# Kernel tuning notes

Hardware: AMD Instinct MI355X
Metric: run time of the kernel (lower is better)

Reference implementation:

```python
import jax, jax.numpy as jnp
import numpy as np

D = 1024
H = 16
FFN = 4096
B = 4
S = 1024
EPS = 1e-12
NEG = -1e9


def _layernorm(x, gamma, beta):
    mean = x.mean(-1, keepdims=True)
    var = ((x - mean) ** 2).mean(-1, keepdims=True)  # biased var, matches unbiased=False
    return gamma * (x - mean) * jax.lax.rsqrt(var + EPS) + beta


def setup_inputs() -> dict:
    key = jax.random.key(0)
    ks = jax.random.split(key, 16)
    s_in = 1.0 / np.sqrt(D)
    s_ff = 1.0 / np.sqrt(FFN)
    return {
        "x": jax.random.normal(ks[0], (B, S, D), dtype=jnp.float32),
        "mask": jax.random.randint(ks[1], (B, H, S), 0, 2) > 0,  # bernoulli(0.5) key mask
        "Wqkv": jax.random.uniform(ks[2], (3 * D, D), minval=-s_in, maxval=s_in),
        "bqkv": jax.random.uniform(ks[3], (3 * D,), minval=-s_in, maxval=s_in),
        "Wo": jax.random.uniform(ks[4], (D, D), minval=-s_in, maxval=s_in),
        "bo": jax.random.uniform(ks[5], (D,), minval=-s_in, maxval=s_in),
        "W1": jax.random.uniform(ks[6], (FFN, D), minval=-s_in, maxval=s_in),
        "b1": jax.random.uniform(ks[7], (FFN,), minval=-s_in, maxval=s_in),
        "W2": jax.random.uniform(ks[8], (D, FFN), minval=-s_ff, maxval=s_ff),
        "b2": jax.random.uniform(ks[9], (D,), minval=-s_ff, maxval=s_ff),
        "g1": jnp.ones((D,), jnp.float32),
        "be1": jnp.zeros((D,), jnp.float32),
        "g2": jnp.ones((D,), jnp.float32),
        "be2": jnp.zeros((D,), jnp.float32),
    }


def reference(x, mask, Wqkv, bqkv, Wo, bo, W1, b1, W2, b2, g1, be1, g2, be2):
    b, s, _ = x.shape
    hd = D // H
    scale = hd ** -0.5

    # --- ProbSparseSelfAttention (dropout in eval mode) ---
    qkv = x @ Wqkv.T + bqkv                                   # [b, s, 3D]
    q, k, v = jnp.split(qkv, 3, axis=-1)
    q = q.reshape(b, s, H, hd).transpose(0, 2, 1, 3)          # [b, h, s, d]
    k = k.reshape(b, s, H, hd).transpose(0, 2, 1, 3)
    v = v.reshape(b, s, H, hd).transpose(0, 2, 1, 3)
    scores = jnp.einsum('bhid,bhjd->bhij', q * scale, k)      # [b, h, s, s]
    scores = jnp.where(mask[:, :, None, :], scores, NEG)      # mask keys (broadcast over i)
    attn = jax.nn.softmax(scores, axis=-1)
    ctx = jnp.einsum('bhij,bhjd->bhid', attn, v)
    ctx = ctx.transpose(0, 2, 1, 3).reshape(b, s, D)
    attn_out = ctx @ Wo.T + bo

    # residual + LayerNorm 1
    h = _layernorm(attn_out + x, g1, be1)

    # --- FFN ---
    ff = jax.nn.relu(h @ W1.T + b1) @ W2.T + b2

    # residual + LayerNorm 2
    return _layernorm(ff + h, g2, be2)
```

## Files before the change

### kernel.cpp

```cpp
#include <hip/hip_runtime.h>

#define DDIM 1024
#define FFN_DIM 4096
#define SS 1024
#define MTOK 4096

typedef __bf16 bf16x8 __attribute__((ext_vector_type(8)));
typedef float f32x4 __attribute__((ext_vector_type(4)));
typedef unsigned short ushort4v __attribute__((ext_vector_type(4)));
typedef unsigned short ushort8v __attribute__((ext_vector_type(8)));

__device__ __forceinline__ unsigned short f2bf(float f) {
    union { float f; unsigned u; } x;
    x.f = f;
    unsigned r = x.u + 0x7FFFu + ((x.u >> 16) & 1u);
    return (unsigned short)(r >> 16);
}

__device__ __forceinline__ int swz(int off) {
    return off ^ ((((off >> 7) & 7) ^ ((off >> 10) & 1)) << 4);
}

__device__ __forceinline__ void gload_lds16(const void* g, void* l) {
    __builtin_amdgcn_global_load_lds(
        (__attribute__((address_space(1))) unsigned int*)(unsigned long long)(g),
        (__attribute__((address_space(3))) unsigned int*)(l), 16, 0, 0);
}

__global__ __launch_bounds__(256) void cvt_bf16(const float* __restrict__ in,
                                                unsigned short* __restrict__ out, int n4) {
    int i = blockIdx.x * 256 + threadIdx.x;
    if (i < n4) {
        float4 v = ((const float4*)in)[i];
        ushort4v u = {f2bf(v.x), f2bf(v.y), f2bf(v.z), f2bf(v.w)};
        ((ushort4v*)out)[i] = u;
    }
}

template <int EPI, int BN>
__global__ __launch_bounds__(256) void gemm_bt(const unsigned short* __restrict__ A,
                                               const unsigned short* __restrict__ B,
                                               const float* __restrict__ bias,
                                               void* __restrict__ Cout,
                                               int M, int N, int K) {
    constexpr int NF = BN / 32;
    __shared__ unsigned short Asm[128 * 32];
    __shared__ unsigned short Bsm[BN * 32];
    const int tid = threadIdx.x;
    const int wid = tid >> 6, lane = tid & 63;
    const int m0 = blockIdx.y * 128, n0 = blockIdx.x * BN;
    const int lr = lane & 15, lk = (lane >> 4) * 8;
    const int wr = (wid >> 1) * 64, wc = (wid & 1) * (BN / 2);

    f32x4 acc[4][NF];
#pragma unroll
    for (int i = 0; i < 4; i++)
#pragma unroll
        for (int j = 0; j < NF; j++) acc[i][j] = (f32x4){0.f, 0.f, 0.f, 0.f};

    const unsigned short* Ag = A + (size_t)m0 * K;
    const unsigned short* Bg = B + (size_t)n0 * K;

    for (int k0 = 0; k0 < K; k0 += 32) {
#pragma unroll
        for (int p = 0; p < 2; ++p) {
            int idx = p * 4096 + wid * 1024 + lane * 16;
            int row = idx >> 6, ce = (idx & 63) >> 1;
            gload_lds16(Ag + (size_t)row * K + k0 + ce, (char*)Asm + p * 4096 + wid * 1024);
        }
#pragma unroll
        for (int p = 0; p < BN / 64; ++p) {
            int idx = p * 4096 + wid * 1024 + lane * 16;
            int row = idx >> 6, ce = (idx & 63) >> 1;
            gload_lds16(Bg + (size_t)row * K + k0 + ce, (char*)Bsm + p * 4096 + wid * 1024);
        }
        __syncthreads();
        bf16x8 af[4], bfr[NF];
#pragma unroll
        for (int m = 0; m < 4; m++) af[m] = *(const bf16x8*)&Asm[(wr + m * 16 + lr) * 32 + lk];
#pragma unroll
        for (int n = 0; n < NF; n++) bfr[n] = *(const bf16x8*)&Bsm[(wc + n * 16 + lr) * 32 + lk];
#pragma unroll
        for (int m = 0; m < 4; m++)
#pragma unroll
            for (int n = 0; n < NF; n++)
                acc[m][n] = __builtin_amdgcn_mfma_f32_16x16x32_bf16(af[m], bfr[n], acc[m][n], 0, 0, 0);
        __syncthreads();
    }

    float bv[NF];
#pragma unroll
    for (int n = 0; n < NF; n++) bv[n] = bias[n0 + wc + n * 16 + lr];
    const int r0 = (lane >> 4) * 4;
#pragma unroll
    for (int m = 0; m < 4; m++) {
#pragma unroll
        for (int n = 0; n < NF; n++) {
            int col = n0 + wc + n * 16 + lr;
#pragma unroll
            for (int r = 0; r < 4; r++) {
                int row = m0 + wr + m * 16 + r0 + r;
                float v = acc[m][n][r] + bv[n];
                if (EPI == 0) {
                    ((float*)Cout)[(size_t)row * N + col] = v;
                } else if (EPI == 1) {
                    ((unsigned short*)Cout)[(size_t)row * N + col] = f2bf(v);
                } else {
                    ((unsigned short*)Cout)[(size_t)row * N + col] = f2bf(fmaxf(v, 0.f));
                }
            }
        }
    }
}

__global__ __launch_bounds__(256) void vtrans(const unsigned short* __restrict__ qkv,
                                              unsigned short* __restrict__ vt) {
    __shared__ unsigned short T[64 * 64];
    const int tid = threadIdx.x;
    const int bh = blockIdx.y, b = bh >> 4, h = bh & 15;
    const int s0 = blockIdx.x * 64;
    const unsigned short* src = qkv + (size_t)(b * SS + s0) * 3072 + 2048 + h * 64;
#pragma unroll
    for (int p = 0; p < 2; p++) {
        int idx = p * 4096 + tid * 16;
        int row = idx >> 7, ce = (idx & 127) >> 1;
        ushort8v v = *(const ushort8v*)(src + (size_t)row * 3072 + ce);
        *(ushort8v*)((char*)T + swz(idx)) = v;
    }
    __syncthreads();
    unsigned short* dst = vt + (size_t)bh * 64 * SS + s0;
#pragma unroll
    for (int p = 0; p < 2; p++) {
        int idx = p * 4096 + tid * 16;
        int d = idx >> 7, t0 = (idx & 127) >> 1;
        ushort8v o;
#pragma unroll
        for (int i = 0; i < 8; i++)
            o[i] = *(const unsigned short*)((char*)T + swz((t0 + i) * 128 + d * 2));
        *(ushort8v*)(dst + (size_t)d * SS + t0) = o;
    }
}

__global__ __launch_bounds__(256) void attn_fused(const unsigned short* __restrict__ qkv,
                                                  const unsigned short* __restrict__ vt,
                                                  const int* __restrict__ mask,
                                                  unsigned short* __restrict__ ctx) {
    __shared__ unsigned short Ksm[2][64 * 64];
    __shared__ unsigned short Vsm[2][64 * 64];
    __shared__ unsigned short Psm[4][16 * 64];
    __shared__ float maskadd[2][64];
    const int tid = threadIdx.x, wid = tid >> 6, lane = tid & 63;
    const int bh = blockIdx.y, b = bh >> 4, h = bh & 15;
    const int q0 = blockIdx.x * 64;
    const int lr = lane & 15, lk2 = (lane >> 4) * 16;
    const size_t base = (size_t)b * SS * 3072 + h * 64;

    bf16x8 qf[2];
    {
        const unsigned short* qp = qkv + base + (size_t)(q0 + wid * 16 + lr) * 3072;
        qf[0] = *(const bf16x8*)(qp + (lk2 >> 1));
        qf[1] = *(const bf16x8*)(qp + 32 + (lk2 >> 1));
    }
    float m_run[4] = {-3e38f, -3e38f, -3e38f, -3e38f};
    float l_run[4] = {0.f, 0.f, 0.f, 0.f};
    f32x4 oacc[4];
#pragma unroll
    for (int i = 0; i < 4; i++) oacc[i] = (f32x4){0.f, 0.f, 0.f, 0.f};

    const unsigned short* Kgb = qkv + base + 1024;
    const unsigned short* Vgb = vt + (size_t)bh * 64 * SS;

    auto stage = [&](int buf, int kt) {
#pragma unroll
        for (int p = 0; p < 2; p++) {
            int idx = p * 4096 + wid * 1024 + lane * 16;
            int s = swz(idx);
            int row = s >> 7, ce = (s & 127) >> 1;
            gload_lds16(Kgb + (size_t)(kt * 64 + row) * 3072 + ce,
                        (char*)Ksm[buf] + p * 4096 + wid * 1024);
            gload_lds16(Vgb + (size_t)row * SS + kt * 64 + ce,
                        (char*)Vsm[buf] + p * 4096 + wid * 1024);
        }
        if (tid < 64) maskadd[buf][tid] = mask[bh * SS + kt * 64 + tid] ? 0.f : -1e9f;
    };

    stage(0, 0);
    for (int kt = 0; kt < SS / 64; ++kt) {
        const int cur = kt & 1;
        __syncthreads();
        if (kt < SS / 64 - 1) stage(cur ^ 1, kt + 1);
        const char* Kb = (const char*)Ksm[cur];
        const char* Vb = (const char*)Vsm[cur];

        f32x4 sc[4];
#pragma unroll
        for (int nt = 0; nt < 4; nt++) {
            f32x4 a = (f32x4){0.f, 0.f, 0.f, 0.f};
            int rowb = (nt * 16 + lr) * 128;
            bf16x8 k0v = *(const bf16x8*)(Kb + swz(rowb + lk2));
            bf16x8 k1v = *(const bf16x8*)(Kb + swz(rowb + 64 + lk2));
            a = __builtin_amdgcn_mfma_f32_16x16x32_bf16(qf[0], k0v, a, 0, 0, 0);
            a = __builtin_amdgcn_mfma_f32_16x16x32_bf16(qf[1], k1v, a, 0, 0, 0);
            sc[nt] = a;
        }
        float mk[4];
#pragma unroll
        for (int nt = 0; nt < 4; nt++) mk[nt] = maskadd[cur][nt * 16 + lr];
#pragma unroll
        for (int r = 0; r < 4; r++) {
            float v = -3e38f;
#pragma unroll
            for (int nt = 0; nt < 4; nt++) {
                float s = sc[nt][r] * 0.125f + mk[nt];
                sc[nt][r] = s;
                v = fmaxf(v, s);
            }
            v = fmaxf(v, __shfl_xor(v, 1));
            v = fmaxf(v, __shfl_xor(v, 2));
            v = fmaxf(v, __shfl_xor(v, 4));
            v = fmaxf(v, __shfl_xor(v, 8));
            float mnew = fmaxf(m_run[r], v);
            float alpha = __expf(m_run[r] - mnew);
            m_run[r] = mnew;
            float ls = 0.f;
#pragma unroll
            for (int nt = 0; nt < 4; nt++) {
                float pexp = __expf(sc[nt][r] - mnew);
                sc[nt][r] = pexp;
                ls += pexp;
            }
            ls += __shfl_xor(ls, 1);
            ls += __shfl_xor(ls, 2);
            ls += __shfl_xor(ls, 4);
            ls += __shfl_xor(ls, 8);
            l_run[r] = l_run[r] * alpha + ls;
#pragma unroll
            for (int dt = 0; dt < 4; dt++) oacc[dt][r] *= alpha;
        }
        const int prow = (lane >> 4) * 4;
        char* Pb = (char*)Psm[wid];
#pragma unroll
        for (int nt = 0; nt < 4; nt++)
#pragma unroll
            for (int r = 0; r < 4; r++)
                *(unsigned short*)(Pb + swz((prow + r) * 128 + (nt * 16 + lr) * 2)) = f2bf(sc[nt][r]);
        bf16x8 pf0 = *(const bf16x8*)(Pb + swz(lr * 128 + lk2));
        bf16x8 pf1 = *(const bf16x8*)(Pb + swz(lr * 128 + 64 + lk2));
#pragma unroll
        for (int dt = 0; dt < 4; dt++) {
            int rowb = (dt * 16 + lr) * 128;
            bf16x8 v0 = *(const bf16x8*)(Vb + swz(rowb + lk2));
            bf16x8 v1 = *(const bf16x8*)(Vb + swz(rowb + 64 + lk2));
            oacc[dt] = __builtin_amdgcn_mfma_f32_16x16x32_bf16(pf0, v0, oacc[dt], 0, 0, 0);
            oacc[dt] = __builtin_amdgcn_mfma_f32_16x16x32_bf16(pf1, v1, oacc[dt], 0, 0, 0);
        }
    }
#pragma unroll
    for (int dt = 0; dt < 4; dt++) {
#pragma unroll
        for (int r = 0; r < 4; r++) {
            float v = oacc[dt][r] / l_run[r];
            int row = q0 + wid * 16 + (lane >> 4) * 4 + r;
            ctx[(size_t)(b * SS + row) * DDIM + h * 64 + dt * 16 + lr] = f2bf(v);
        }
    }
}

__global__ __launch_bounds__(256) void resid_ln(const float* __restrict__ a,
                                                const float* __restrict__ b,
                                                const float* __restrict__ gamma,
                                                const float* __restrict__ beta,
                                                float* __restrict__ of32,
                                                unsigned short* __restrict__ obf) {
    __shared__ float red[16];
    const int row = blockIdx.x, tid = threadIdx.x;
    const int wid = tid >> 6, lane = tid & 63;
    float4 av = ((const float4*)(a + (size_t)row * DDIM))[tid];
    float4 bv = ((const float4*)(b + (size_t)row * DDIM))[tid];
    float4 v;
    v.x = av.x + bv.x; v.y = av.y + bv.y; v.z = av.z + bv.z; v.w = av.w + bv.w;
    float s = v.x + v.y + v.z + v.w;
    float s2 = v.x * v.x + v.y * v.y + v.z * v.z + v.w * v.w;
#pragma unroll
    for (int off = 1; off < 64; off <<= 1) {
        s += __shfl_xor(s, off);
        s2 += __shfl_xor(s2, off);
    }
    if (lane == 0) { red[wid] = s; red[8 + wid] = s2; }
    __syncthreads();
    s = red[0] + red[1] + red[2] + red[3];
    s2 = red[8] + red[9] + red[10] + red[11];
    float mean = s * (1.f / 1024.f);
    float var = s2 * (1.f / 1024.f) - mean * mean;
    float rstd = rsqrtf(var + 1e-12f);
    float4 g = ((const float4*)gamma)[tid];
    float4 be = ((const float4*)beta)[tid];
    float4 o;
    o.x = g.x * (v.x - mean) * rstd + be.x;
    o.y = g.y * (v.y - mean) * rstd + be.y;
    o.z = g.z * (v.z - mean) * rstd + be.z;
    o.w = g.w * (v.w - mean) * rstd + be.w;
    if (of32) ((float4*)(of32 + (size_t)row * DDIM))[tid] = o;
    if (obf) {
        ushort4v u = {f2bf(o.x), f2bf(o.y), f2bf(o.z), f2bf(o.w)};
        ((ushort4v*)(obf + (size_t)row * DDIM))[tid] = u;
    }
}

extern "C" void kernel_launch(void* const* d_in, const int* in_sizes, int n_in,
                              void* d_out, int out_size, void* d_ws, size_t ws_size,
                              hipStream_t stream) {
    const float* x    = (const float*)d_in[0];
    const int*   mask = (const int*)d_in[1];
    const float* Wqkv = (const float*)d_in[2];
    const float* bqkv = (const float*)d_in[3];
    const float* Wo   = (const float*)d_in[4];
    const float* bo   = (const float*)d_in[5];
    const float* W1   = (const float*)d_in[6];
    const float* b1   = (const float*)d_in[7];
    const float* W2   = (const float*)d_in[8];
    const float* b2   = (const float*)d_in[9];
    const float* g1   = (const float*)d_in[10];
    const float* be1  = (const float*)d_in[11];
    const float* g2   = (const float*)d_in[12];
    const float* be2  = (const float*)d_in[13];
    float* out = (float*)d_out;

    char* ws = (char*)d_ws;
    unsigned short* xbf   = (unsigned short*)(ws + 0);
    unsigned short* vtb   = (unsigned short*)(ws + 0);
    unsigned short* ff1   = (unsigned short*)(ws + 0);
    unsigned short* qkvbf = (unsigned short*)(ws + (8ull << 20));
    unsigned short* ctx   = (unsigned short*)(ws + (32ull << 20));
    unsigned short* wqkvb = (unsigned short*)(ws + (40ull << 20));
    unsigned short* wob   = (unsigned short*)(ws + (46ull << 20));
    unsigned short* w1b   = (unsigned short*)(ws + (48ull << 20));
    unsigned short* w2b   = (unsigned short*)(ws + (56ull << 20));
    float* attno          = (float*)(ws + (64ull << 20));
    float* ff2            = (float*)(ws + (64ull << 20));
    float* hf             = (float*)(ws + (80ull << 20));
    unsigned short* hbf   = (unsigned short*)(ws + (96ull << 20));

    cvt_bf16<<<4096, 256, 0, stream>>>(x, xbf, 1048576);
    cvt_bf16<<<3072, 256, 0, stream>>>(Wqkv, wqkvb, 786432);
    cvt_bf16<<<1024, 256, 0, stream>>>(Wo, wob, 262144);
    cvt_bf16<<<4096, 256, 0, stream>>>(W1, w1b, 1048576);
    cvt_bf16<<<4096, 256, 0, stream>>>(W2, w2b, 1048576);

    gemm_bt<1, 128><<<dim3(24, 32), 256, 0, stream>>>(xbf, wqkvb, bqkv, qkvbf, MTOK, 3072, 1024);
    vtrans<<<dim3(16, 64), 256, 0, stream>>>(qkvbf, vtb);
    attn_fused<<<dim3(16, 64), 256, 0, stream>>>(qkvbf, vtb, mask, ctx);
    gemm_bt<0, 64><<<dim3(16, 32), 256, 0, stream>>>(ctx, wob, bo, attno, MTOK, 1024, 1024);
    resid_ln<<<4096, 256, 0, stream>>>(attno, x, g1, be1, hf, hbf);
    gemm_bt<2, 128><<<dim3(32, 32), 256, 0, stream>>>(hbf, w1b, b1, ff1, MTOK, FFN_DIM, 1024);
    gemm_bt<0, 64><<<dim3(16, 32), 256, 0, stream>>>(ff1, w2b, b2, ff2, MTOK, 1024, FFN_DIM);
    resid_ln<<<4096, 256, 0, stream>>>(ff2, hf, g2, be2, out, nullptr);
}
```

Baseline: 415.2 us.

## Double-buffer GEMM LDS tiles, split-K FFN2, bf16 intermediates between GEMM and LayerNorm

The GEMM kernel gets double-buffered LDS so the next k-tile's global-to-LDS loads are issued before the MFMAs on the current tile, which removes one barrier per iteration. Block size is fixed at 128x128. The FFN down-projection is split along K into two partial bf16 outputs, and the second LayerNorm sums them with the residual. GEMM outputs and the residual h are now stored as bf16 instead of fp32, which cuts memory traffic but adds rounding error to the residual path. The Wo GEMM now launches only 256 blocks, so each block does more work and some CUs may sit idle.

Result: faster. 382.1 us (-8.0%).

```diff
diff --git a/kernel.cpp b/kernel.cpp
--- a/kernel.cpp
+++ b/kernel.cpp
@@ -15,6 +15,11 @@
     x.f = f;
     unsigned r = x.u + 0x7FFFu + ((x.u >> 16) & 1u);
     return (unsigned short)(r >> 16);
+}
+__device__ __forceinline__ float bf2f(unsigned short u) {
+    union { unsigned u; float f; } x;
+    x.u = (unsigned)u << 16;
+    return x.f;
 }
 
 __device__ __forceinline__ int swz(int off) {
@@ -37,77 +42,76 @@
     }
 }
 
-template <int EPI, int BN>
+template <int EPI, int SPLITK>
 __global__ __launch_bounds__(256) void gemm_bt(const unsigned short* __restrict__ A,
                                                const unsigned short* __restrict__ B,
                                                const float* __restrict__ bias,
-                                               void* __restrict__ Cout,
+                                               unsigned short* __restrict__ Cout,
                                                int M, int N, int K) {
-    constexpr int NF = BN / 32;
-    __shared__ unsigned short Asm[128 * 32];
-    __shared__ unsigned short Bsm[BN * 32];
+    __shared__ unsigned short Asm[2][128 * 32];
+    __shared__ unsigned short Bsm[2][128 * 32];
     const int tid = threadIdx.x;
     const int wid = tid >> 6, lane = tid & 63;
-    const int m0 = blockIdx.y * 128, n0 = blockIdx.x * BN;
+    const int m0 = blockIdx.y * 128, n0 = blockIdx.x * 128;
     const int lr = lane & 15, lk = (lane >> 4) * 8;
-    const int wr = (wid >> 1) * 64, wc = (wid & 1) * (BN / 2);
-
-    f32x4 acc[4][NF];
+    const int wr = (wid >> 1) * 64, wc = (wid & 1) * 64;
+    const int Kper = K / SPLITK;
+    const int kbase = blockIdx.z * Kper;
+    const int nkt = Kper / 32;
+
+    f32x4 acc[4][4];
 #pragma unroll
     for (int i = 0; i < 4; i++)
 #pragma unroll
-        for (int j = 0; j < NF; j++) acc[i][j] = (f32x4){0.f, 0.f, 0.f, 0.f};
+        for (int j = 0; j < 4; j++) acc[i][j] = (f32x4){0.f, 0.f, 0.f, 0.f};
 
     const unsigned short* Ag = A + (size_t)m0 * K;
     const unsigned short* Bg = B + (size_t)n0 * K;
 
-    for (int k0 = 0; k0 < K; k0 += 32) {
+    auto stage = [&](int buf, int k0) {
 #pragma unroll
         for (int p = 0; p < 2; ++p) {
             int idx = p * 4096 + wid * 1024 + lane * 16;
             int row = idx >> 6, ce = (idx & 63) >> 1;
-            gload_lds16(Ag + (size_t)row * K + k0 + ce, (char*)Asm + p * 4096 + wid * 1024);
-        }
-#pragma unroll
-        for (int p = 0; p < BN / 64; ++p) {
-            int idx = p * 4096 + wid * 1024 + lane * 16;
-            int row = idx >> 6, ce = (idx & 63) >> 1;
-            gload_lds16(Bg + (size_t)row * K + k0 + ce, (char*)Bsm + p * 4096 + wid * 1024);
-        }
+            gload_lds16(Ag + (size_t)row * K + k0 + ce, (char*)Asm[buf] + p * 4096 + wid * 1024);
+            gload_lds16(Bg + (size_t)row * K + k0 + ce, (char*)Bsm[buf] + p * 4096 + wid * 1024);
+        }
+    };
+
+    stage(0, kbase);
+    for (int kt = 0; kt < nkt; ++kt) {
+        const int cur = kt & 1;
         __syncthreads();
-        bf16x8 af[4], bfr[NF];
-#pragma unroll
-        for (int m = 0; m < 4; m++) af[m] = *(const bf16x8*)&Asm[(wr + m * 16 + lr) * 32 + lk];
-#pragma unroll
-        for (int n = 0; n < NF; n++) bfr[n] = *(const bf16x8*)&Bsm[(wc + n * 16 + lr) * 32 + lk];
+        if (kt + 1 < nkt) stage(cur ^ 1, kbase + (kt + 1) * 32);
+        bf16x8 af[4], bfr[4];
+#pragma unroll
+        for (int m = 0; m < 4; m++) af[m] = *(const bf16x8*)&Asm[cur][(wr + m * 16 + lr) * 32 + lk];
+#pragma unroll
+        for (int n = 0; n < 4; n++) bfr[n] = *(const bf16x8*)&Bsm[cur][(wc + n * 16 + lr) * 32 + lk];
 #pragma unroll
         for (int m = 0; m < 4; m++)
 #pragma unroll
-            for (int n = 0; n < NF; n++)
+            for (int n = 0; n < 4; n++)
                 acc[m][n] = __builtin_amdgcn_mfma_f32_16x16x32_bf16(af[m], bfr[n], acc[m][n], 0, 0, 0);
-        __syncthreads();
-    }
-
-    float bv[NF];
-#pragma unroll
-    for (int n = 0; n < NF; n++) bv[n] = bias[n0 + wc + n * 16 + lr];
+    }
+
+    unsigned short* Op = Cout + (size_t)blockIdx.z * M * N;
+    float bv[4];
+    const bool hasb = (SPLITK == 1) || (blockIdx.z == 0);
+#pragma unroll
+    for (int n = 0; n < 4; n++) bv[n] = hasb ? bias[n0 + wc + n * 16 + lr] : 0.f;
     const int r0 = (lane >> 4) * 4;
 #pragma unroll
     for (int m = 0; m < 4; m++) {
 #pragma unroll
-        for (int n = 0; n < NF; n++) {
+        for (int n = 0; n < 4; n++) {
             int col = n0 + wc + n * 16 + lr;
 #pragma unroll
             for (int r = 0; r < 4; r++) {
                 int row = m0 + wr + m * 16 + r0 + r;
                 float v = acc[m][n][r] + bv[n];
-                if (EPI == 0) {
-                    ((float*)Cout)[(size_t)row * N + col] = v;
-                } else if (EPI == 1) {
-                    ((unsigned short*)Cout)[(size_t)row * N + col] = f2bf(v);
-                } else {
-                    ((unsigned short*)Cout)[(size_t)row * N + col] = f2bf(fmaxf(v, 0.f));
-                }
+                if (EPI == 2) v = fmaxf(v, 0.f);
+                Op[(size_t)row * N + col] = f2bf(v);
             }
         }
     }
@@ -266,26 +270,60 @@
     }
 }
 
-__global__ __launch_bounds__(256) void resid_ln(const float* __restrict__ a,
-                                                const float* __restrict__ b,
-                                                const float* __restrict__ gamma,
-                                                const float* __restrict__ beta,
-                                                float* __restrict__ of32,
-                                                unsigned short* __restrict__ obf) {
+__global__ __launch_bounds__(256) void resid_ln1(const unsigned short* __restrict__ attno,
+                                                 const float* __restrict__ x,
+                                                 const float* __restrict__ gamma,
+                                                 const float* __restrict__ beta,
+                                                 unsigned short* __restrict__ hbf) {
     __shared__ float red[16];
     const int row = blockIdx.x, tid = threadIdx.x;
     const int wid = tid >> 6, lane = tid & 63;
-    float4 av = ((const float4*)(a + (size_t)row * DDIM))[tid];
-    float4 bv = ((const float4*)(b + (size_t)row * DDIM))[tid];
+    ushort4v av = ((const ushort4v*)(attno + (size_t)row * DDIM))[tid];
+    float4 bv = ((const float4*)(x + (size_t)row * DDIM))[tid];
     float4 v;
-    v.x = av.x + bv.x; v.y = av.y + bv.y; v.z = av.z + bv.z; v.w = av.w + bv.w;
+    v.x = bf2f(av[0]) + bv.x; v.y = bf2f(av[1]) + bv.y;
+    v.z = bf2f(av[2]) + bv.z; v.w = bf2f(av[3]) + bv.w;
     float s = v.x + v.y + v.z + v.w;
     float s2 = v.x * v.x + v.y * v.y + v.z * v.z + v.w * v.w;
 #pragma unroll
-    for (int off = 1; off < 64; off <<= 1) {
-        s += __shfl_xor(s, off);
-        s2 += __shfl_xor(s2, off);
-    }
+    for (int off = 1; off < 64; off <<= 1) { s += __shfl_xor(s, off); s2 += __shfl_xor(s2, off); }
+    if (lane == 0) { red[wid] = s; red[8 + wid] = s2; }
+    __syncthreads();
+    s = red[0] + red[1] + red[2] + red[3];
+    s2 = red[8] + red[9] + red[10] + red[11];
+    float mean = s * (1.f / 1024.f);
+    float var = s2 * (1.f / 1024.f) - mean * mean;
+    float rstd = rsqrtf(var + 1e-12f);
+    float4 g = ((const float4*)gamma)[tid];
+    float4 be = ((const float4*)beta)[tid];
+    ushort4v u = {f2bf(g.x * (v.x - mean) * rstd + be.x),
+                  f2bf(g.y * (v.y - mean) * rstd + be.y),
+                  f2bf(g.z * (v.z - mean) * rstd + be.z),
+                  f2bf(g.w * (v.w - mean) * rstd + be.w)};
+    ((ushort4v*)(hbf + (size_t)row * DDIM))[tid] = u;
+}
+
+__global__ __launch_bounds__(256) void resid_ln2(const unsigned short* __restrict__ p0,
+                                                 const unsigned short* __restrict__ p1,
+                                                 const unsigned short* __restrict__ hbf,
+                                                 const float* __restrict__ gamma,
+                                                 const float* __restrict__ beta,
+                                                 float* __restrict__ out) {
+    __shared__ float red[16];
+    const int row = blockIdx.x, tid = threadIdx.x;
+    const int wid = tid >> 6, lane = tid & 63;
+    ushort4v a0 = ((const ushort4v*)(p0 + (size_t)row * DDIM))[tid];
+    ushort4v a1 = ((const ushort4v*)(p1 + (size_t)row * DDIM))[tid];
+    ushort4v hv = ((const ushort4v*)(hbf + (size_t)row * DDIM))[tid];
+    float4 v;
+    v.x = bf2f(a0[0]) + bf2f(a1[0]) + bf2f(hv[0]);
+    v.y = bf2f(a0[1]) + bf2f(a1[1]) + bf2f(hv[1]);
+    v.z = bf2f(a0[2]) + bf2f(a1[2]) + bf2f(hv[2]);
+    v.w = bf2f(a0[3]) + bf2f(a1[3]) + bf2f(hv[3]);
+    float s = v.x + v.y + v.z + v.w;
+    float s2 = v.x * v.x + v.y * v.y + v.z * v.z + v.w * v.w;
+#pragma unroll
+    for (int off = 1; off < 64; off <<= 1) { s += __shfl_xor(s, off); s2 += __shfl_xor(s2, off); }
     if (lane == 0) { red[wid] = s; red[8 + wid] = s2; }
     __syncthreads();
     s = red[0] + red[1] + red[2] + red[3];
@@ -300,11 +338,7 @@
     o.y = g.y * (v.y - mean) * rstd + be.y;
     o.z = g.z * (v.z - mean) * rstd + be.z;
     o.w = g.w * (v.w - mean) * rstd + be.w;
-    if (of32) ((float4*)(of32 + (size_t)row * DDIM))[tid] = o;
-    if (obf) {
-        ushort4v u = {f2bf(o.x), f2bf(o.y), f2bf(o.z), f2bf(o.w)};
-        ((ushort4v*)(obf + (size_t)row * DDIM))[tid] = u;
-    }
+    ((float4*)(out + (size_t)row * DDIM))[tid] = o;
 }
 
 extern "C" void kernel_launch(void* const* d_in, const int* in_sizes, int n_in,
@@ -329,17 +363,16 @@
     char* ws = (char*)d_ws;
     unsigned short* xbf   = (unsigned short*)(ws + 0);
     unsigned short* vtb   = (unsigned short*)(ws + 0);
-    unsigned short* ff1   = (unsigned short*)(ws + 0);
     unsigned short* qkvbf = (unsigned short*)(ws + (8ull << 20));
+    unsigned short* ff1   = (unsigned short*)(ws + (8ull << 20));
     unsigned short* ctx   = (unsigned short*)(ws + (32ull << 20));
-    unsigned short* wqkvb = (unsigned short*)(ws + (40ull << 20));
-    unsigned short* wob   = (unsigned short*)(ws + (46ull << 20));
-    unsigned short* w1b   = (unsigned short*)(ws + (48ull << 20));
-    unsigned short* w2b   = (unsigned short*)(ws + (56ull << 20));
-    float* attno          = (float*)(ws + (64ull << 20));
-    float* ff2            = (float*)(ws + (64ull << 20));
-    float* hf             = (float*)(ws + (80ull << 20));
-    unsigned short* hbf   = (unsigned short*)(ws + (96ull << 20));
+    unsigned short* w1b   = (unsigned short*)(ws + (40ull << 20));
+    unsigned short* w2b   = (unsigned short*)(ws + (48ull << 20));
+    unsigned short* wqkvb = (unsigned short*)(ws + (56ull << 20));
+    unsigned short* wob   = (unsigned short*)(ws + (62ull << 20));
+    unsigned short* attno = (unsigned short*)(ws + (64ull << 20));
+    unsigned short* hbf   = (unsigned short*)(ws + (72ull << 20));
+    unsigned short* pff   = (unsigned short*)(ws + (80ull << 20));
 
     cvt_bf16<<<4096, 256, 0, stream>>>(x, xbf, 1048576);
     cvt_bf16<<<3072, 256, 0, stream>>>(Wqkv, wqkvb, 786432);
@@ -347,12 +380,12 @@
     cvt_bf16<<<4096, 256, 0, stream>>>(W1, w1b, 1048576);
     cvt_bf16<<<4096, 256, 0, stream>>>(W2, w2b, 1048576);
 
-    gemm_bt<1, 128><<<dim3(24, 32), 256, 0, stream>>>(xbf, wqkvb, bqkv, qkvbf, MTOK, 3072, 1024);
+    gemm_bt<1, 1><<<dim3(24, 32), 256, 0, stream>>>(xbf, wqkvb, bqkv, qkvbf, MTOK, 3072, 1024);
     vtrans<<<dim3(16, 64), 256, 0, stream>>>(qkvbf, vtb);
     attn_fused<<<dim3(16, 64), 256, 0, stream>>>(qkvbf, vtb, mask, ctx);
-    gemm_bt<0, 64><<<dim3(16, 32), 256, 0, stream>>>(ctx, wob, bo, attno, MTOK, 1024, 1024);
-    resid_ln<<<4096, 256, 0, stream>>>(attno, x, g1, be1, hf, hbf);
-    gemm_bt<2, 128><<<dim3(32, 32), 256, 0, stream>>>(hbf, w1b, b1, ff1, MTOK, FFN_DIM, 1024);
-    gemm_bt<0, 64><<<dim3(16, 32), 256, 0, stream>>>(ff1, w2b, b2, ff2, MTOK, 1024, FFN_DIM);
-    resid_ln<<<4096, 256, 0, stream>>>(ff2, hf, g2, be2, out, nullptr);
-}
+    gemm_bt<1, 1><<<dim3(8, 32), 256, 0, stream>>>(ctx, wob, bo, attno, MTOK, 1024, 1024);
+    resid_ln1<<<4096, 256, 0, stream>>>(attno, x, g1, be1, hbf);
+    gemm_bt<2, 1><<<dim3(32, 32), 256, 0, stream>>>(hbf, w1b, b1, ff1, MTOK, FFN_DIM, 1024);
+    gemm_bt<1, 2><<<dim3(8, 32, 2), 256, 0, stream>>>(ff1, w2b, b2, pff, MTOK, 1024, FFN_DIM);
+    resid_ln2<<<4096, 256, 0, stream>>>(pff, pff + (size_t)MTOK * DDIM, hbf, g2, be2, out);
+}
```
